# Kernel tuning notes

Hardware: AMD Instinct MI355X
Metric: run time of the kernel (lower is better)

Reference implementation:

```python
import jax, jax.numpy as jnp
import numpy as np

K = 5          # lbp kernel_size (odd)
POOL = 2       # pool_size
C = 64         # input channels
B, H, W = 8, 256, 256
OUT_CH = 1
NEG_SLOPE = 0.01
LN_EPS = 1e-5


def _idx_pairs(k):
    pairs = [([0, i], [k - 1, k - 1 - i]) for i in range(k)]
    pairs += [([i, k - 1], [k - 1 - i, 0]) for i in range(1, k - 1)]
    return pairs  # 2K-2 pairs


def setup_inputs() -> dict:
    key = jax.random.key(0)
    k1, k2, k3 = jax.random.split(key, 3)
    x = jax.random.normal(k1, (B, C, H, W), dtype=jnp.float32)
    m = 2 * K - 2
    conv_w = jax.random.normal(k2, (OUT_CH, m), dtype=jnp.float32) / np.float32(np.sqrt(m))
    conv_b = jax.random.normal(k3, (OUT_CH,), dtype=jnp.float32) * 0.01
    return {"x": x, "conv_w": conv_w, "conv_b": conv_b}


def _avg_pool(x):
    # torch avg_pool2d(kernel=POOL, stride=1, padding=POOL//2, count_include_pad=True)
    p = POOL // 2
    s = jax.lax.reduce_window(x, jnp.float32(0.0), jax.lax.add,
                              (1, 1, POOL, POOL), (1, 1, 1, 1),
                              ((0, 0), (0, 0), (p, p), (p, p)))
    return s / jnp.float32(POOL * POOL)


def reference(x, conv_w, conv_b):
    xp = _avg_pool(x)                 # [B, C, H+1, W+1]
    # Each lbp kernel plane is (+1 center, -1 at offset) replicated over all C
    # input channels, so the conv reduces to shifts of the channel sum.
    xs = xp.sum(axis=1)               # [B, H', W']
    pad = K // 2
    Hp, Wp = xs.shape[-2], xs.shape[-1]
    xs_pad = jnp.pad(xs, ((0, 0), (pad, pad), (pad, pad)))

    def shift(rc):
        r, c = rc
        return xs_pad[:, r:r + Hp, c:c + Wp]

    # (conv even ch) - (conv odd ch) = shift(idx1) - shift(idx0)
    feats = jnp.stack([shift(b) - shift(a) for a, b in _idx_pairs(K)], axis=1)  # [B, 2K-2, H', W']
    y = jnp.einsum('bmhw,om->bohw', feats, conv_w) + conv_b[None, :, None, None]
    # layer_norm over last two dims, no affine
    mu = y.mean(axis=(-2, -1), keepdims=True)
    var = ((y - mu) ** 2).mean(axis=(-2, -1), keepdims=True)
    y = (y - mu) / jnp.sqrt(var + LN_EPS)
    return jnp.where(y >= 0, y, NEG_SLOPE * y)
```

## Files before the change

### kernel.cpp

```cpp
#include <hip/hip_runtime.h>
#include <math.h>

#define BB 8
#define CC 64
#define HH 256
#define WW 256
#define HP 257
#define PADW 261
#define NPB (HP * HP)
#define NBLK ((NPB + 255) / 256)

#define OFF_PART 0
#define OFF_STATS (2 * BB * NBLK)
#define OFF_S 4352
#define OFF_XSP (OFF_S + BB * HH * WW)

__global__ __launch_bounds__(256) void k_chansum(const float* __restrict__ x,
                                                 float* __restrict__ s) {
    int idx = blockIdx.x * 256 + threadIdx.x;
    int b = idx >> 14;
    int p = idx & 16383;
    const float4* xp = reinterpret_cast<const float4*>(x)
                       + (size_t)b * (CC * 16384) + p;
    float4 acc = make_float4(0.f, 0.f, 0.f, 0.f);
#pragma unroll 16
    for (int c = 0; c < CC; ++c) {
        float4 v = xp[(size_t)c * 16384];
        acc.x += v.x; acc.y += v.y; acc.z += v.z; acc.w += v.w;
    }
    reinterpret_cast<float4*>(s)[idx] = acc;
}

__global__ __launch_bounds__(256) void k_pool(const float* __restrict__ s,
                                              float* __restrict__ xsp) {
    int idx = blockIdx.x * 256 + threadIdx.x;
    if (idx >= BB * PADW * PADW) return;
    int b = idx / (PADW * PADW);
    int rem = idx % (PADW * PADW);
    int r = rem / PADW, cc = rem % PADW;
    float v = 0.f;
    if (r >= 2 && r < 2 + HP && cc >= 2 && cc < 2 + HP) {
        int i = r - 2, j = cc - 2;
        const float* sb = s + b * (HH * WW);
        float v00 = (i >= 1      && j >= 1)      ? sb[(i - 1) * WW + (j - 1)] : 0.f;
        float v01 = (i >= 1      && j <= WW - 1) ? sb[(i - 1) * WW + j]       : 0.f;
        float v10 = (i <= HH - 1 && j >= 1)      ? sb[i * WW + (j - 1)]       : 0.f;
        float v11 = (i <= HH - 1 && j <= WW - 1) ? sb[i * WW + j]             : 0.f;
        v = 0.25f * (v00 + v01 + v10 + v11);
    }
    xsp[idx] = v;
}

__device__ __forceinline__ float conv_y(const float* __restrict__ xb, int h, int w,
                                        const float* __restrict__ cw, float cb) {
    const float* p = xb + h * PADW + w;
    float y = cb;
    y -= cw[0] * p[0 * PADW + 0] + cw[1] * p[0 * PADW + 1] + cw[2] * p[0 * PADW + 2]
       + cw[3] * p[0 * PADW + 3] + cw[4] * p[0 * PADW + 4];
    y += cw[4] * p[4 * PADW + 0] + cw[3] * p[4 * PADW + 1] + cw[2] * p[4 * PADW + 2]
       + cw[1] * p[4 * PADW + 3] + cw[0] * p[4 * PADW + 4];
    y -= cw[5] * p[1 * PADW + 4] + cw[6] * p[2 * PADW + 4] + cw[7] * p[3 * PADW + 4];
    y += cw[7] * p[1 * PADW + 0] + cw[6] * p[2 * PADW + 0] + cw[5] * p[3 * PADW + 0];
    return y;
}

__global__ __launch_bounds__(256) void k_conv_part(const float* __restrict__ xsp,
                                                   const float* __restrict__ cw,
                                                   const float* __restrict__ cbp,
                                                   float* __restrict__ ws) {
    int b = blockIdx.y;
    int e = blockIdx.x * 256 + threadIdx.x;
    float y = 0.f;
    if (e < NPB) {
        int h = e / HP, w = e % HP;
        y = conv_y(xsp + b * (PADW * PADW), h, w, cw, cbp[0]);
    }
    float v1 = y, v2 = y * y;
    for (int off = 32; off > 0; off >>= 1) {
        v1 += __shfl_down(v1, off);
        v2 += __shfl_down(v2, off);
    }
    __shared__ float red[8];
    int lane = threadIdx.x & 63, wid = threadIdx.x >> 6;
    if (lane == 0) { red[wid] = v1; red[4 + wid] = v2; }
    __syncthreads();
    if (threadIdx.x == 0) {
        float s1 = red[0] + red[1] + red[2] + red[3];
        float s2 = red[4] + red[5] + red[6] + red[7];
        ws[OFF_PART + b * NBLK + blockIdx.x] = s1;
        ws[OFF_PART + BB * NBLK + b * NBLK + blockIdx.x] = s2;
    }
}

__global__ __launch_bounds__(256) void k_stats(float* __restrict__ ws) {
    int b = blockIdx.x;
    float v1 = 0.f, v2 = 0.f;
    for (int i = threadIdx.x; i < NBLK; i += 256) {
        v1 += ws[OFF_PART + b * NBLK + i];
        v2 += ws[OFF_PART + BB * NBLK + b * NBLK + i];
    }
    for (int off = 32; off > 0; off >>= 1) {
        v1 += __shfl_down(v1, off);
        v2 += __shfl_down(v2, off);
    }
    __shared__ float red[8];
    int lane = threadIdx.x & 63, wid = threadIdx.x >> 6;
    if (lane == 0) { red[wid] = v1; red[4 + wid] = v2; }
    __syncthreads();
    if (threadIdx.x == 0) {
        float s1 = red[0] + red[1] + red[2] + red[3];
        float s2 = red[4] + red[5] + red[6] + red[7];
        float mu = s1 / (float)NPB;
        float var = s2 / (float)NPB - mu * mu;
        float rsig = 1.0f / sqrtf(var + 1e-5f);
        ws[OFF_STATS + b] = mu;
        ws[OFF_STATS + 8 + b] = rsig;
    }
}

__global__ __launch_bounds__(256) void k_final(const float* __restrict__ xsp,
                                               const float* __restrict__ cw,
                                               const float* __restrict__ cbp,
                                               const float* __restrict__ ws,
                                               float* __restrict__ out) {
    int b = blockIdx.y;
    int e = blockIdx.x * 256 + threadIdx.x;
    if (e >= NPB) return;
    int h = e / HP, w = e % HP;
    float y = conv_y(xsp + b * (PADW * PADW), h, w, cw, cbp[0]);
    float mu = ws[OFF_STATS + b];
    float rsig = ws[OFF_STATS + 8 + b];
    float z = (y - mu) * rsig;
    out[b * NPB + e] = (z >= 0.f) ? z : 0.01f * z;
}

extern "C" void kernel_launch(void* const* d_in, const int* in_sizes, int n_in,
                              void* d_out, int out_size, void* d_ws, size_t ws_size,
                              hipStream_t stream) {
    const float* x  = (const float*)d_in[0];
    const float* cw = (const float*)d_in[1];
    const float* cb = (const float*)d_in[2];
    float* out = (float*)d_out;
    float* ws  = (float*)d_ws;
    float* s   = ws + OFF_S;
    float* xsp = ws + OFF_XSP;

    k_chansum<<<(BB * HH * WW / 4) / 256, 256, 0, stream>>>(x, s);
    k_pool<<<(BB * PADW * PADW + 255) / 256, 256, 0, stream>>>(s, xsp);
    dim3 g3(NBLK, BB);
    k_conv_part<<<g3, 256, 0, stream>>>(xsp, cw, cb, ws);
    k_stats<<<BB, 256, 0, stream>>>(ws);
    k_final<<<g3, 256, 0, stream>>>(xsp, cw, cb, ws, out);
}
```

Before: 204.7 us.

## Fold avg-pool into combined 6x6 stencil, write padded sums, fuse stats into final

```diff
diff --git a/kernel.cpp b/kernel.cpp
--- a/kernel.cpp
+++ b/kernel.cpp
@@ -6,74 +6,103 @@
 #define HH 256
 #define WW 256
 #define HP 257
-#define PADW 261
 #define NPB (HP * HP)
 #define NBLK ((NPB + 255) / 256)
 
+#define SROWS 262
+#define SSTR  264
+#define SPIMG (SROWS * SSTR)
+
 #define OFF_PART 0
-#define OFF_STATS (2 * BB * NBLK)
-#define OFF_S 4352
-#define OFF_XSP (OFF_S + BB * HH * WW)
+#define OFF_Y    4352
+#define OFF_SPAD (OFF_Y + BB * NPB)
+
+#define N_INT (BB * 16384)
+#define PAD_PER_IMG 908
+#define N_TOT (N_INT + BB * PAD_PER_IMG)
 
 __global__ __launch_bounds__(256) void k_chansum(const float* __restrict__ x,
-                                                 float* __restrict__ s) {
-    int idx = blockIdx.x * 256 + threadIdx.x;
-    int b = idx >> 14;
-    int p = idx & 16383;
-    const float4* xp = reinterpret_cast<const float4*>(x)
-                       + (size_t)b * (CC * 16384) + p;
-    float4 acc = make_float4(0.f, 0.f, 0.f, 0.f);
+                                                 float* __restrict__ ws) {
+    int tid = blockIdx.x * 256 + threadIdx.x;
+    float4* sp4 = reinterpret_cast<float4*>(ws + OFF_SPAD);
+    if (tid < N_INT) {
+        int b = tid >> 14;
+        int p = tid & 16383;
+        int i = p >> 6;
+        int j4 = p & 63;
+        const float4* xp = reinterpret_cast<const float4*>(x)
+                           + (size_t)b * (CC * 16384) + p;
+        float4 acc = make_float4(0.f, 0.f, 0.f, 0.f);
 #pragma unroll 16
-    for (int c = 0; c < CC; ++c) {
-        float4 v = xp[(size_t)c * 16384];
-        acc.x += v.x; acc.y += v.y; acc.z += v.z; acc.w += v.w;
+        for (int c = 0; c < CC; ++c) {
+            float4 v = xp[(size_t)c * 16384];
+            acc.x += v.x; acc.y += v.y; acc.z += v.z; acc.w += v.w;
+        }
+        sp4[b * (SPIMG / 4) + (i + 3) * (SSTR / 4) + 1 + j4] = acc;
+    } else {
+        int j = tid - N_INT;
+        if (j < BB * PAD_PER_IMG) {
+            int img = j / PAD_PER_IMG;
+            int k = j % PAD_PER_IMG;
+            int row, col4;
+            if (k < 396) {
+                int r = k / 66;
+                row = (r < 3) ? r : 256 + r;
+                col4 = k % 66;
+            } else {
+                int k2 = k - 396;
+                row = 3 + (k2 >> 1);
+                col4 = (k2 & 1) ? 65 : 0;
+            }
+            sp4[img * (SPIMG / 4) + row * (SSTR / 4) + col4] =
+                make_float4(0.f, 0.f, 0.f, 0.f);
+        }
     }
-    reinterpret_cast<float4*>(s)[idx] = acc;
 }
 
-__global__ __launch_bounds__(256) void k_pool(const float* __restrict__ s,
-                                              float* __restrict__ xsp) {
-    int idx = blockIdx.x * 256 + threadIdx.x;
-    if (idx >= BB * PADW * PADW) return;
-    int b = idx / (PADW * PADW);
-    int rem = idx % (PADW * PADW);
-    int r = rem / PADW, cc = rem % PADW;
-    float v = 0.f;
-    if (r >= 2 && r < 2 + HP && cc >= 2 && cc < 2 + HP) {
-        int i = r - 2, j = cc - 2;
-        const float* sb = s + b * (HH * WW);
-        float v00 = (i >= 1      && j >= 1)      ? sb[(i - 1) * WW + (j - 1)] : 0.f;
-        float v01 = (i >= 1      && j <= WW - 1) ? sb[(i - 1) * WW + j]       : 0.f;
-        float v10 = (i <= HH - 1 && j >= 1)      ? sb[i * WW + (j - 1)]       : 0.f;
-        float v11 = (i <= HH - 1 && j <= WW - 1) ? sb[i * WW + j]             : 0.f;
-        v = 0.25f * (v00 + v01 + v10 + v11);
-    }
-    xsp[idx] = v;
+__device__ __forceinline__ void build_w(const float* __restrict__ cw, float W[6][6]) {
+    float T[5][5];
+#pragma unroll
+    for (int i = 0; i < 5; ++i)
+#pragma unroll
+        for (int j = 0; j < 5; ++j) T[i][j] = 0.f;
+#pragma unroll
+    for (int d = 0; d < 5; ++d) { T[0][d] = -cw[d]; T[4][d] = cw[4 - d]; }
+    T[1][4] = -cw[5]; T[2][4] = -cw[6]; T[3][4] = -cw[7];
+    T[1][0] =  cw[7]; T[2][0] =  cw[6]; T[3][0] =  cw[5];
+#pragma unroll
+    for (int u = 0; u < 6; ++u)
+#pragma unroll
+        for (int v = 0; v < 6; ++v) {
+            float a = 0.f;
+#pragma unroll
+            for (int dr = u - 1; dr <= u; ++dr)
+#pragma unroll
+                for (int dc = v - 1; dc <= v; ++dc)
+                    if (dr >= 0 && dr < 5 && dc >= 0 && dc < 5) a += T[dr][dc];
+            W[u][v] = 0.25f * a;
+        }
 }
 
-__device__ __forceinline__ float conv_y(const float* __restrict__ xb, int h, int w,
-                                        const float* __restrict__ cw, float cb) {
-    const float* p = xb + h * PADW + w;
-    float y = cb;
-    y -= cw[0] * p[0 * PADW + 0] + cw[1] * p[0 * PADW + 1] + cw[2] * p[0 * PADW + 2]
-       + cw[3] * p[0 * PADW + 3] + cw[4] * p[0 * PADW + 4];
-    y += cw[4] * p[4 * PADW + 0] + cw[3] * p[4 * PADW + 1] + cw[2] * p[4 * PADW + 2]
-       + cw[1] * p[4 * PADW + 3] + cw[0] * p[4 * PADW + 4];
-    y -= cw[5] * p[1 * PADW + 4] + cw[6] * p[2 * PADW + 4] + cw[7] * p[3 * PADW + 4];
-    y += cw[7] * p[1 * PADW + 0] + cw[6] * p[2 * PADW + 0] + cw[5] * p[3 * PADW + 0];
-    return y;
-}
-
-__global__ __launch_bounds__(256) void k_conv_part(const float* __restrict__ xsp,
-                                                   const float* __restrict__ cw,
-                                                   const float* __restrict__ cbp,
-                                                   float* __restrict__ ws) {
+__global__ __launch_bounds__(256) void k_conv(float* __restrict__ ws,
+                                              const float* __restrict__ cw,
+                                              const float* __restrict__ cbp) {
     int b = blockIdx.y;
     int e = blockIdx.x * 256 + threadIdx.x;
+    float W[6][6];
+    build_w(cw, W);
     float y = 0.f;
     if (e < NPB) {
         int h = e / HP, w = e % HP;
-        y = conv_y(xsp + b * (PADW * PADW), h, w, cw, cbp[0]);
+        const float* p = ws + OFF_SPAD + b * SPIMG + h * SSTR + w + 1;
+        float acc = cbp[0];
+#pragma unroll
+        for (int u = 0; u < 6; ++u)
+#pragma unroll
+            for (int v = 0; v < 6; ++v)
+                acc += W[u][v] * p[u * SSTR + v];
+        y = acc;
+        ws[OFF_Y + b * NPB + e] = y;
     }
     float v1 = y, v2 = y * y;
     for (int off = 32; off > 0; off >>= 1) {
@@ -85,15 +114,15 @@
     if (lane == 0) { red[wid] = v1; red[4 + wid] = v2; }
     __syncthreads();
     if (threadIdx.x == 0) {
-        float s1 = red[0] + red[1] + red[2] + red[3];
-        float s2 = red[4] + red[5] + red[6] + red[7];
-        ws[OFF_PART + b * NBLK + blockIdx.x] = s1;
-        ws[OFF_PART + BB * NBLK + b * NBLK + blockIdx.x] = s2;
+        ws[OFF_PART + b * NBLK + blockIdx.x] = red[0] + red[1] + red[2] + red[3];
+        ws[OFF_PART + BB * NBLK + b * NBLK + blockIdx.x] =
+            red[4] + red[5] + red[6] + red[7];
     }
 }
 
-__global__ __launch_bounds__(256) void k_stats(float* __restrict__ ws) {
-    int b = blockIdx.x;
+__global__ __launch_bounds__(256) void k_final(const float* __restrict__ ws,
+                                               float* __restrict__ out) {
+    int b = blockIdx.y;
     float v1 = 0.f, v2 = 0.f;
     for (int i = threadIdx.x; i < NBLK; i += 256) {
         v1 += ws[OFF_PART + b * NBLK + i];
@@ -104,6 +133,7 @@
         v2 += __shfl_down(v2, off);
     }
     __shared__ float red[8];
+    __shared__ float st[2];
     int lane = threadIdx.x & 63, wid = threadIdx.x >> 6;
     if (lane == 0) { red[wid] = v1; red[4 + wid] = v2; }
     __syncthreads();
@@ -112,26 +142,16 @@
         float s2 = red[4] + red[5] + red[6] + red[7];
         float mu = s1 / (float)NPB;
         float var = s2 / (float)NPB - mu * mu;
-        float rsig = 1.0f / sqrtf(var + 1e-5f);
-        ws[OFF_STATS + b] = mu;
-        ws[OFF_STATS + 8 + b] = rsig;
+        st[0] = mu;
+        st[1] = 1.0f / sqrtf(var + 1e-5f);
     }
-}
-
-__global__ __launch_bounds__(256) void k_final(const float* __restrict__ xsp,
-                                               const float* __restrict__ cw,
-                                               const float* __restrict__ cbp,
-                                               const float* __restrict__ ws,
-                                               float* __restrict__ out) {
-    int b = blockIdx.y;
+    __syncthreads();
+    float mu = st[0], rs = st[1];
     int e = blockIdx.x * 256 + threadIdx.x;
-    if (e >= NPB) return;
-    int h = e / HP, w = e % HP;
-    float y = conv_y(xsp + b * (PADW * PADW), h, w, cw, cbp[0]);
-    float mu = ws[OFF_STATS + b];
-    float rsig = ws[OFF_STATS + 8 + b];
-    float z = (y - mu) * rsig;
-    out[b * NPB + e] = (z >= 0.f) ? z : 0.01f * z;
+    if (e < NPB) {
+        float z = (ws[OFF_Y + b * NPB + e] - mu) * rs;
+        out[b * NPB + e] = (z >= 0.f) ? z : 0.01f * z;
+    }
 }
 
 extern "C" void kernel_launch(void* const* d_in, const int* in_sizes, int n_in,
@@ -142,13 +162,9 @@
     const float* cb = (const float*)d_in[2];
     float* out = (float*)d_out;
     float* ws  = (float*)d_ws;
-    float* s   = ws + OFF_S;
-    float* xsp = ws + OFF_XSP;
 
-    k_chansum<<<(BB * HH * WW / 4) / 256, 256, 0, stream>>>(x, s);
-    k_pool<<<(BB * PADW * PADW + 255) / 256, 256, 0, stream>>>(s, xsp);
-    dim3 g3(NBLK, BB);
-    k_conv_part<<<g3, 256, 0, stream>>>(xsp, cw, cb, ws);
-    k_stats<<<BB, 256, 0, stream>>>(ws);
-    k_final<<<g3, 256, 0, stream>>>(xsp, cw, cb, ws, out);
+    k_chansum<<<(N_TOT + 255) / 256, 256, 0, stream>>>(x, ws);
+    dim3 g(NBLK, BB);
+    k_conv<<<g, 256, 0, stream>>>(ws, cw, cb);
+    k_final<<<g, 256, 0, stream>>>(ws, out);
 }
```

After: 202.3 us. No clear change (-1.2%).
